# Optimization experiments

Measured on AMD Instinct MI355X. Metric: run time of the kernel, lower is better.

Reference implementation:

```python
import jax, jax.numpy as jnp
import numpy as np

# ---- init_kwargs-derived constants ----
B, IN_F, OUT_F = 8192, 4096, 4096
W_SCALE = 0.01          # layer_params['w_scale']
B_SCALE = 0.01          # layer_params['b_scale']
IN_MIN, IN_MAX = -1.0, 1.0   # input_stats
NUM_BITS = 8
QMAX = 2 ** NUM_BITS - 1
IN_SCALE = (IN_MAX - IN_MIN) / QMAX
IN_ZP = int(round(-IN_MIN / (IN_SCALE + 1e-12)))


def setup_inputs() -> dict:
    key = jax.random.key(0)
    k1, k2, k3 = jax.random.split(key, 3)
    x_float = jax.random.normal(k1, (B, IN_F), dtype=jnp.float32)
    # int8-range weights/bias (stored as int32 containers)
    w_q = jax.random.randint(k2, (OUT_F, IN_F), -128, 128, dtype=jnp.int32)
    b_q = jax.random.randint(k3, (OUT_F,), -128, 128, dtype=jnp.int32)
    return {"x_float": x_float, "w_q": w_q, "b_q": b_q}


def reference(x_float, w_q, b_q):
    # quantize input to uint8 range [0,255]
    x_q = jnp.clip(jnp.round(x_float / IN_SCALE + IN_ZP), 0, 255).astype(jnp.int32)
    x_shifted = x_q - IN_ZP                       # [B, IN_F] int32
    # exact int32 accumulation matmul: [B, IN_F] @ [IN_F, OUT_F]
    acc_int = jnp.matmul(x_shifted, w_q.T, preferred_element_type=jnp.int32)
    out = acc_int.astype(jnp.float32) * (IN_SCALE * W_SCALE)
    out = out + b_q.astype(jnp.float32) * B_SCALE  # bias_float = b_q * b_scale
    return out
```

## Files before the change

### kernel.cpp

```cpp
#include <hip/hip_runtime.h>
#include <stdint.h>

constexpr int Mdim = 8192;
constexpr int Ndim = 4096;
constexpr int Kdim = 4096;
constexpr int NT = Kdim / 128;

#define ISF        ((float)(2.0 / 255.0))
#define OUT_SCALE  ((float)(2.0 / 255.0 * 0.01))
#define BSCALE     0.01f

typedef int i32x4 __attribute__((ext_vector_type(4)));

__global__ __launch_bounds__(256) void quantize_x(const float* __restrict__ x,
                                                  int* __restrict__ x8,
                                                  int ngroups) {
  int idx = blockIdx.x * 256 + threadIdx.x;
  int stride = gridDim.x * 256;
  for (int g = idx; g < ngroups; g += stride) {
    float4 v = reinterpret_cast<const float4*>(x)[g];
    int a0 = (int)rintf(v.x / ISF + 127.0f);
    int a1 = (int)rintf(v.y / ISF + 127.0f);
    int a2 = (int)rintf(v.z / ISF + 127.0f);
    int a3 = (int)rintf(v.w / ISF + 127.0f);
    a0 = a0 < 0 ? 0 : (a0 > 255 ? 255 : a0); a0 -= 128;
    a1 = a1 < 0 ? 0 : (a1 > 255 ? 255 : a1); a1 -= 128;
    a2 = a2 < 0 ? 0 : (a2 > 255 ? 255 : a2); a2 -= 128;
    a3 = a3 < 0 ? 0 : (a3 > 255 ? 255 : a3); a3 -= 128;
    x8[g] = (a0 & 0xff) | ((a1 & 0xff) << 8) | ((a2 & 0xff) << 16) |
            (int)(((unsigned)(a3 & 0xff)) << 24);
  }
}

__global__ __launch_bounds__(256) void convert_w(const int* __restrict__ wq,
                                                 int* __restrict__ w8,
                                                 int* __restrict__ wsum) {
  int row = blockIdx.x;
  const int4* src = reinterpret_cast<const int4*>(wq + (size_t)row * Kdim);
  int* dst = w8 + (size_t)row * (Kdim / 4);
  int s = 0;
#pragma unroll
  for (int i = 0; i < 4; ++i) {
    int idx = i * 256 + threadIdx.x;
    int4 v = src[idx];
    s += v.x + v.y + v.z + v.w;
    dst[idx] = (v.x & 0xff) | ((v.y & 0xff) << 8) | ((v.z & 0xff) << 16) |
               (int)(((unsigned)(v.w & 0xff)) << 24);
  }
  __shared__ int red[256];
  red[threadIdx.x] = s;
  __syncthreads();
  for (int off = 128; off; off >>= 1) {
    if ((int)threadIdx.x < off) red[threadIdx.x] += red[threadIdx.x + off];
    __syncthreads();
  }
  if (threadIdx.x == 0) wsum[row] = red[0];
}

#define AS1C const __attribute__((address_space(1))) void*
#define AS3  __attribute__((address_space(3))) void*
#define GLL(src, dst) __builtin_amdgcn_global_load_lds((AS1C)(src), (AS3)(dst), 16, 0, 0)
#define BAR() asm volatile("s_barrier" ::: "memory")
#define MFMA(a, b, c) __builtin_amdgcn_mfma_i32_16x16x64_i8(a, b, c, 0, 0, 0)

__global__ __launch_bounds__(512) void gemm_i8_8ph(const int8_t* __restrict__ A8,
                                                   const int8_t* __restrict__ B8,
                                                   const int* __restrict__ wsum,
                                                   const int* __restrict__ bq,
                                                   float* __restrict__ out) {
  __shared__ uint8_t lds[131072];

  int bid = blockIdx.x;
  int wg = (bid & 7) * 64 + (bid >> 3);
  int bm = wg >> 4;
  int bn = wg & 15;

  const int tid = threadIdx.x;
  const int lane = tid & 63;
  const int wv = tid >> 6;
  const int wr = wv >> 2;
  const int wc = wv & 3;
  const int l15 = lane & 15, hi = lane >> 4;

  const int r3 = lane >> 3, s3 = lane & 7;
  const int swcol = (s3 ^ r3) << 4;
  const size_t aoff = (size_t)(bm * 256 + wv * 8 + r3) * Kdim + swcol;
  const size_t boff = (size_t)(bn * 256 + wv * 8 + r3) * Kdim + swcol;
  const int ldsw = wv * 1024;

#define ISSUE_A(P, t, half) do { \
    GLL(A8 + aoff + (size_t)(t) * 128 + (size_t)((half) * 128) * Kdim, \
        &lds[(P) * 32768 + (half) * 16384 + ldsw]); \
    GLL(A8 + aoff + (size_t)(t) * 128 + (size_t)((half) * 128 + 64) * Kdim, \
        &lds[(P) * 32768 + (half) * 16384 + 8192 + ldsw]); \
  } while (0)
#define ISSUE_B(P, t, half) do { \
    GLL(B8 + boff + (size_t)(t) * 128 + (size_t)((half) * 128) * Kdim, \
        &lds[65536 + (P) * 32768 + (half) * 16384 + ldsw]); \
    GLL(B8 + boff + (size_t)(t) * 128 + (size_t)((half) * 128 + 64) * Kdim, \
        &lds[65536 + (P) * 32768 + (half) * 16384 + 8192 + ldsw]); \
  } while (0)

  const int aRow = (wr * 128 + l15) * 128;
  const int bRow = (wc * 64 + l15) * 128;
  const int sl0 = (hi ^ (l15 & 7)) << 4;
  const int sl1 = ((4 + hi) ^ (l15 & 7)) << 4;

#define LDA(P, i, ks) (*reinterpret_cast<const i32x4*>( \
    &lds[(P) * 32768 + aRow + (i) * 2048 + ((ks) ? sl1 : sl0)]))
#define LDB(P, j, ks) (*reinterpret_cast<const i32x4*>( \
    &lds[65536 + (P) * 32768 + bRow + (j) * 2048 + ((ks) ? sl1 : sl0)]))

  i32x4 acc[8][4];
#pragma unroll
  for (int i = 0; i < 8; ++i)
#pragma unroll
    for (int j = 0; j < 4; ++j) acc[i][j] = (i32x4){0, 0, 0, 0};

  ISSUE_A(0, 0, 0); ISSUE_A(0, 0, 1);
  ISSUE_B(0, 0, 0); ISSUE_B(0, 0, 1);
  ISSUE_A(1, 1, 0); ISSUE_A(1, 1, 1);
  asm volatile("s_waitcnt vmcnt(4)" ::: "memory");
  BAR();

#define KTILE(P, t, DOB, DOA, VM4, VM0) do { \
    i32x4 a0[8], a1[8], bb0, bb1; \
     \
    if (DOB) ISSUE_B((P) ^ 1, (t) + 1, 0); \
    bb0 = LDB(P, 0, 0); bb1 = LDB(P, 1, 0); \
    _Pragma("unroll") for (int i = 0; i < 8; ++i) a0[i] = LDA(P, i, 0); \
    BAR(); __builtin_amdgcn_s_setprio(1); \
    _Pragma("unroll") for (int i = 0; i < 8; ++i) { \
      acc[i][0] = MFMA(a0[i], bb0, acc[i][0]); acc[i][1] = MFMA(a0[i], bb1, acc[i][1]); } \
    __builtin_amdgcn_s_setprio(0); BAR(); \
     \
    if (DOB) ISSUE_B((P) ^ 1, (t) + 1, 1); \
    bb0 = LDB(P, 2, 0); bb1 = LDB(P, 3, 0); \
    _Pragma("unroll") for (int i = 0; i < 8; ++i) a1[i] = LDA(P, i, 1); \
    BAR(); __builtin_amdgcn_s_setprio(1); \
    _Pragma("unroll") for (int i = 0; i < 8; ++i) { \
      acc[i][2] = MFMA(a0[i], bb0, acc[i][2]); acc[i][3] = MFMA(a0[i], bb1, acc[i][3]); } \
    __builtin_amdgcn_s_setprio(0); BAR(); \
     \
    if (DOA) ISSUE_A(P, (t) + 2, 0); \
    bb0 = LDB(P, 0, 1); bb1 = LDB(P, 1, 1); \
    BAR(); __builtin_amdgcn_s_setprio(1); \
    _Pragma("unroll") for (int i = 0; i < 8; ++i) { \
      acc[i][0] = MFMA(a1[i], bb0, acc[i][0]); acc[i][1] = MFMA(a1[i], bb1, acc[i][1]); } \
    __builtin_amdgcn_s_setprio(0); BAR(); \
     \
    if (DOA) ISSUE_A(P, (t) + 2, 1); \
    bb0 = LDB(P, 2, 1); bb1 = LDB(P, 3, 1); \
    BAR(); __builtin_amdgcn_s_setprio(1); \
    _Pragma("unroll") for (int i = 0; i < 8; ++i) { \
      acc[i][2] = MFMA(a1[i], bb0, acc[i][2]); acc[i][3] = MFMA(a1[i], bb1, acc[i][3]); } \
    __builtin_amdgcn_s_setprio(0); \
    if (VM4) asm volatile("s_waitcnt vmcnt(4)" ::: "memory"); \
    if (VM0) asm volatile("s_waitcnt vmcnt(0)" ::: "memory"); \
    BAR(); \
  } while (0)

  for (int it = 0; it < NT / 2 - 1; ++it) {
    int ta = 2 * it, tb = 2 * it + 1;
    KTILE(0, ta, 1, 1, 1, 0);
    KTILE(1, tb, 1, 1, 1, 0);
  }
  KTILE(0, 30, 1, 0, 0, 1);
  KTILE(1, 31, 0, 0, 0, 0);

#pragma unroll
  for (int j = 0; j < 4; ++j) {
    int col = bn * 256 + wc * 64 + j * 16 + l15;
    float fb = (float)bq[col] * BSCALE;
    int ws = wsum[col];
#pragma unroll
    for (int i = 0; i < 8; ++i) {
      int rbase = bm * 256 + wr * 128 + i * 16 + hi * 4;
#pragma unroll
      for (int p = 0; p < 4; ++p)
        out[(size_t)(rbase + p) * Ndim + col] = (float)(acc[i][j][p] + ws) * OUT_SCALE + fb;
    }
  }
#undef KTILE
#undef ISSUE_A
#undef ISSUE_B
#undef LDA
#undef LDB
}

__global__ void fallback_kernel(const float* __restrict__ x, const int* __restrict__ wq,
                                const int* __restrict__ bq, float* __restrict__ out) {
  int col = blockIdx.x * 16 + (threadIdx.x & 15);
  int row = blockIdx.y * 16 + (threadIdx.x >> 4);
  const float* xr = x + (size_t)row * Kdim;
  const int* wr_ = wq + (size_t)col * Kdim;
  int acc = 0;
  for (int k = 0; k < Kdim; ++k) {
    int v = (int)rintf(xr[k] / ISF + 127.0f);
    v = v < 0 ? 0 : (v > 255 ? 255 : v);
    acc += (v - 127) * wr_[k];
  }
  out[(size_t)row * Ndim + col] = (float)acc * OUT_SCALE + (float)bq[col] * BSCALE;
}

extern "C" void kernel_launch(void* const* d_in, const int* in_sizes, int n_in,
                              void* d_out, int out_size, void* d_ws, size_t ws_size,
                              hipStream_t stream) {
  const float* x = (const float*)d_in[0];
  const int* wq = (const int*)d_in[1];
  const int* bq = (const int*)d_in[2];
  float* out = (float*)d_out;

  const size_t x8_bytes = (size_t)Mdim * Kdim;
  const size_t w8_bytes = (size_t)Ndim * Kdim;
  const size_t ws_need = x8_bytes + w8_bytes + (size_t)Ndim * sizeof(int);

  if (ws_size >= ws_need) {
    int8_t* x8 = (int8_t*)d_ws;
    int8_t* w8 = x8 + x8_bytes;
    int* wsum = (int*)(w8 + w8_bytes);

    quantize_x<<<2048, 256, 0, stream>>>(x, (int*)x8, Mdim * Kdim / 4);
    convert_w<<<Ndim, 256, 0, stream>>>(wq, (int*)w8, wsum);
    gemm_i8_8ph<<<(Mdim / 256) * (Ndim / 256), 512, 0, stream>>>(x8, w8, wsum, bq, out);
  } else {
    dim3 grid(Ndim / 16, Mdim / 16);
    fallback_kernel<<<grid, 256, 0, stream>>>(x, wq, bq, out);
  }
}
```

Before: 179.2 us.

## Switch int8 GEMM to 32x32x32 MFMA tiles with A/B prefetch roles swapped

Replaces the 16x16x64 int8 MFMA with the 32x32x32 variant, so each wave computes 4x2 32x32 tiles instead of 8x4 16x16 tiles. This cuts the number of MFMA issues and LDS fragment loads per K step. The prefetch schedule is also reordered: the next A tile goes to the other buffer and B is refilled two tiles ahead, and a min-blocks launch bound of 2 is added. The epilogue is rewritten for the 32x32 output layout, which gives a different store pattern and a new LDS swizzle indexing across four K sub-steps.

```diff
diff --git a/kernel.cpp b/kernel.cpp
--- a/kernel.cpp
+++ b/kernel.cpp
@@ -11,6 +11,7 @@
 #define BSCALE     0.01f
 
 typedef int i32x4 __attribute__((ext_vector_type(4)));
+typedef int i32x16 __attribute__((ext_vector_type(16)));
 
 __global__ __launch_bounds__(256) void quantize_x(const float* __restrict__ x,
                                                   int* __restrict__ x8,
@@ -61,13 +62,13 @@
 #define AS3  __attribute__((address_space(3))) void*
 #define GLL(src, dst) __builtin_amdgcn_global_load_lds((AS1C)(src), (AS3)(dst), 16, 0, 0)
 #define BAR() asm volatile("s_barrier" ::: "memory")
-#define MFMA(a, b, c) __builtin_amdgcn_mfma_i32_16x16x64_i8(a, b, c, 0, 0, 0)
-
-__global__ __launch_bounds__(512) void gemm_i8_8ph(const int8_t* __restrict__ A8,
-                                                   const int8_t* __restrict__ B8,
-                                                   const int* __restrict__ wsum,
-                                                   const int* __restrict__ bq,
-                                                   float* __restrict__ out) {
+#define MFMA32(a, b, c) __builtin_amdgcn_mfma_i32_32x32x32_i8(a, b, c, 0, 0, 0)
+
+__global__ __launch_bounds__(512, 2) void gemm_i8_32(const int8_t* __restrict__ A8,
+                                                     const int8_t* __restrict__ B8,
+                                                     const int* __restrict__ wsum,
+                                                     const int* __restrict__ bq,
+                                                     float* __restrict__ out) {
   __shared__ uint8_t lds[131072];
 
   int bid = blockIdx.x;
@@ -80,7 +81,8 @@
   const int wv = tid >> 6;
   const int wr = wv >> 2;
   const int wc = wv & 3;
-  const int l15 = lane & 15, hi = lane >> 4;
+  const int l31 = lane & 31, hi1 = lane >> 5;
+  const int sw = l31 & 7;
 
   const int r3 = lane >> 3, s3 = lane & 7;
   const int swcol = (s3 ^ r3) << 4;
@@ -101,59 +103,71 @@
         &lds[65536 + (P) * 32768 + (half) * 16384 + 8192 + ldsw]); \
   } while (0)
 
-  const int aRow = (wr * 128 + l15) * 128;
-  const int bRow = (wc * 64 + l15) * 128;
-  const int sl0 = (hi ^ (l15 & 7)) << 4;
-  const int sl1 = ((4 + hi) ^ (l15 & 7)) << 4;
-
-#define LDA(P, i, ks) (*reinterpret_cast<const i32x4*>( \
-    &lds[(P) * 32768 + aRow + (i) * 2048 + ((ks) ? sl1 : sl0)]))
-#define LDB(P, j, ks) (*reinterpret_cast<const i32x4*>( \
-    &lds[65536 + (P) * 32768 + bRow + (j) * 2048 + ((ks) ? sl1 : sl0)]))
-
-  i32x4 acc[8][4];
-#pragma unroll
-  for (int i = 0; i < 8; ++i)
-#pragma unroll
-    for (int j = 0; j < 4; ++j) acc[i][j] = (i32x4){0, 0, 0, 0};
+  int arow[4], brow[2], sl[4];
+#pragma unroll
+  for (int ri = 0; ri < 4; ++ri) arow[ri] = (wr * 128 + ri * 32 + l31) * 128;
+#pragma unroll
+  for (int cj = 0; cj < 2; ++cj) brow[cj] = (wc * 64 + cj * 32 + l31) * 128;
+#pragma unroll
+  for (int ks = 0; ks < 4; ++ks) sl[ks] = ((ks * 2 + hi1) ^ sw) << 4;
+
+#define LDA(P, ri, ks) (*reinterpret_cast<const i32x4*>(&lds[(P) * 32768 + arow[ri] + sl[ks]]))
+#define LDB(P, cj, ks) (*reinterpret_cast<const i32x4*>(&lds[65536 + (P) * 32768 + brow[cj] + sl[ks]]))
+
+  i32x16 acc[4][2];
+#pragma unroll
+  for (int i = 0; i < 4; ++i)
+#pragma unroll
+    for (int j = 0; j < 2; ++j)
+#pragma unroll
+      for (int p = 0; p < 16; ++p) acc[i][j][p] = 0;
 
   ISSUE_A(0, 0, 0); ISSUE_A(0, 0, 1);
   ISSUE_B(0, 0, 0); ISSUE_B(0, 0, 1);
-  ISSUE_A(1, 1, 0); ISSUE_A(1, 1, 1);
+  ISSUE_B(1, 1, 0); ISSUE_B(1, 1, 1);
   asm volatile("s_waitcnt vmcnt(4)" ::: "memory");
   BAR();
 
-#define KTILE(P, t, DOB, DOA, VM4, VM0) do { \
-    i32x4 a0[8], a1[8], bb0, bb1; \
-     \
-    if (DOB) ISSUE_B((P) ^ 1, (t) + 1, 0); \
-    bb0 = LDB(P, 0, 0); bb1 = LDB(P, 1, 0); \
-    _Pragma("unroll") for (int i = 0; i < 8; ++i) a0[i] = LDA(P, i, 0); \
-    BAR(); __builtin_amdgcn_s_setprio(1); \
-    _Pragma("unroll") for (int i = 0; i < 8; ++i) { \
-      acc[i][0] = MFMA(a0[i], bb0, acc[i][0]); acc[i][1] = MFMA(a0[i], bb1, acc[i][1]); } \
+#define PH_MFMA(AV, BK) do { \
+    acc[0][0] = MFMA32(AV[0], b_[0][BK], acc[0][0]); \
+    acc[0][1] = MFMA32(AV[0], b_[1][BK], acc[0][1]); \
+    acc[1][0] = MFMA32(AV[1], b_[0][BK], acc[1][0]); \
+    acc[1][1] = MFMA32(AV[1], b_[1][BK], acc[1][1]); \
+    acc[2][0] = MFMA32(AV[2], b_[0][BK], acc[2][0]); \
+    acc[2][1] = MFMA32(AV[2], b_[1][BK], acc[2][1]); \
+    acc[3][0] = MFMA32(AV[3], b_[0][BK], acc[3][0]); \
+    acc[3][1] = MFMA32(AV[3], b_[1][BK], acc[3][1]); \
+  } while (0)
+
+#define KTILE(P, t, DOA, DOB, VM4, VM0) do { \
+    i32x4 a_[4], b_[2][4]; \
+     \
+    if (DOA) ISSUE_A((P) ^ 1, (t) + 1, 0); \
+    b_[0][0] = LDB(P, 0, 0); b_[1][0] = LDB(P, 1, 0); \
+    b_[0][1] = LDB(P, 0, 1); b_[1][1] = LDB(P, 1, 1); \
+    a_[0] = LDA(P, 0, 0); a_[1] = LDA(P, 1, 0); a_[2] = LDA(P, 2, 0); a_[3] = LDA(P, 3, 0); \
+    BAR(); __builtin_amdgcn_s_setprio(1); \
+    PH_MFMA(a_, 0); \
     __builtin_amdgcn_s_setprio(0); BAR(); \
      \
-    if (DOB) ISSUE_B((P) ^ 1, (t) + 1, 1); \
-    bb0 = LDB(P, 2, 0); bb1 = LDB(P, 3, 0); \
-    _Pragma("unroll") for (int i = 0; i < 8; ++i) a1[i] = LDA(P, i, 1); \
-    BAR(); __builtin_amdgcn_s_setprio(1); \
-    _Pragma("unroll") for (int i = 0; i < 8; ++i) { \
-      acc[i][2] = MFMA(a0[i], bb0, acc[i][2]); acc[i][3] = MFMA(a0[i], bb1, acc[i][3]); } \
+    if (DOA) ISSUE_A((P) ^ 1, (t) + 1, 1); \
+    b_[0][2] = LDB(P, 0, 2); b_[1][2] = LDB(P, 1, 2); \
+    b_[0][3] = LDB(P, 0, 3); b_[1][3] = LDB(P, 1, 3); \
+    a_[0] = LDA(P, 0, 1); a_[1] = LDA(P, 1, 1); a_[2] = LDA(P, 2, 1); a_[3] = LDA(P, 3, 1); \
+    BAR(); __builtin_amdgcn_s_setprio(1); \
+    PH_MFMA(a_, 1); \
     __builtin_amdgcn_s_setprio(0); BAR(); \
      \
-    if (DOA) ISSUE_A(P, (t) + 2, 0); \
-    bb0 = LDB(P, 0, 1); bb1 = LDB(P, 1, 1); \
-    BAR(); __builtin_amdgcn_s_setprio(1); \
-    _Pragma("unroll") for (int i = 0; i < 8; ++i) { \
-      acc[i][0] = MFMA(a1[i], bb0, acc[i][0]); acc[i][1] = MFMA(a1[i], bb1, acc[i][1]); } \
+    if (DOB) ISSUE_B(P, (t) + 2, 0); \
+    a_[0] = LDA(P, 0, 2); a_[1] = LDA(P, 1, 2); a_[2] = LDA(P, 2, 2); a_[3] = LDA(P, 3, 2); \
+    BAR(); __builtin_amdgcn_s_setprio(1); \
+    PH_MFMA(a_, 2); \
     __builtin_amdgcn_s_setprio(0); BAR(); \
      \
-    if (DOA) ISSUE_A(P, (t) + 2, 1); \
-    bb0 = LDB(P, 2, 1); bb1 = LDB(P, 3, 1); \
-    BAR(); __builtin_amdgcn_s_setprio(1); \
-    _Pragma("unroll") for (int i = 0; i < 8; ++i) { \
-      acc[i][2] = MFMA(a1[i], bb0, acc[i][2]); acc[i][3] = MFMA(a1[i], bb1, acc[i][3]); } \
+    if (DOB) ISSUE_B(P, (t) + 2, 1); \
+    a_[0] = LDA(P, 0, 3); a_[1] = LDA(P, 1, 3); a_[2] = LDA(P, 2, 3); a_[3] = LDA(P, 3, 3); \
+    BAR(); __builtin_amdgcn_s_setprio(1); \
+    PH_MFMA(a_, 3); \
     __builtin_amdgcn_s_setprio(0); \
     if (VM4) asm volatile("s_waitcnt vmcnt(4)" ::: "memory"); \
     if (VM0) asm volatile("s_waitcnt vmcnt(0)" ::: "memory"); \
@@ -161,27 +175,29 @@
   } while (0)
 
   for (int it = 0; it < NT / 2 - 1; ++it) {
-    int ta = 2 * it, tb = 2 * it + 1;
-    KTILE(0, ta, 1, 1, 1, 0);
-    KTILE(1, tb, 1, 1, 1, 0);
+    KTILE(0, 2 * it, 1, 1, 1, 0);
+    KTILE(1, 2 * it + 1, 1, 1, 1, 0);
   }
   KTILE(0, 30, 1, 0, 0, 1);
   KTILE(1, 31, 0, 0, 0, 0);
 
 #pragma unroll
-  for (int j = 0; j < 4; ++j) {
-    int col = bn * 256 + wc * 64 + j * 16 + l15;
+  for (int cj = 0; cj < 2; ++cj) {
+    int col = bn * 256 + wc * 64 + cj * 32 + l31;
     float fb = (float)bq[col] * BSCALE;
     int ws = wsum[col];
 #pragma unroll
-    for (int i = 0; i < 8; ++i) {
-      int rbase = bm * 256 + wr * 128 + i * 16 + hi * 4;
-#pragma unroll
-      for (int p = 0; p < 4; ++p)
-        out[(size_t)(rbase + p) * Ndim + col] = (float)(acc[i][j][p] + ws) * OUT_SCALE + fb;
+    for (int ri = 0; ri < 4; ++ri) {
+      int rb = bm * 256 + wr * 128 + ri * 32 + hi1 * 4;
+#pragma unroll
+      for (int p = 0; p < 16; ++p) {
+        int row = rb + (p & 3) + 8 * (p >> 2);
+        out[(size_t)row * Ndim + col] = (float)(acc[ri][cj][p] + ws) * OUT_SCALE + fb;
+      }
     }
   }
 #undef KTILE
+#undef PH_MFMA
 #undef ISSUE_A
 #undef ISSUE_B
 #undef LDA
@@ -222,7 +238,7 @@
 
     quantize_x<<<2048, 256, 0, stream>>>(x, (int*)x8, Mdim * Kdim / 4);
     convert_w<<<Ndim, 256, 0, stream>>>(wq, (int*)w8, wsum);
-    gemm_i8_8ph<<<(Mdim / 256) * (Ndim / 256), 512, 0, stream>>>(x8, w8, wsum, bq, out);
+    gemm_i8_32<<<(Mdim / 256) * (Ndim / 256), 512, 0, stream>>>(x8, w8, wsum, bq, out);
   } else {
     dim3 grid(Ndim / 16, Mdim / 16);
     fallback_kernel<<<grid, 256, 0, stream>>>(x, wq, bq, out);
```

Result: slower. 193.4 us (+7.9%).

## Software-pipeline LDS fragment loads across MFMA phases and tiles

Applied to the files above, without the earlier changes.

Restructures the int8 GEMM main loop so that each phase's LDS reads for the next B/A fragments are issued before the current phase's MFMAs, and the first fragments of the next K-tile are prefetched inside the last phase. This cuts the barrier count per tile and moves both A-half global-to-LDS issues to the end of the tile, aiming to hide LDS latency behind matrix work. It also adds a min-blocks-per-CU hint of 2 to the launch bounds. With 128 KB of shared memory per block two blocks may not fit on a CU anyway, and the hint could cap registers enough to spill the large accumulator and fragment arrays.

```diff
diff --git a/kernel.cpp b/kernel.cpp
--- a/kernel.cpp
+++ b/kernel.cpp
@@ -61,13 +61,14 @@
 #define AS3  __attribute__((address_space(3))) void*
 #define GLL(src, dst) __builtin_amdgcn_global_load_lds((AS1C)(src), (AS3)(dst), 16, 0, 0)
 #define BAR() asm volatile("s_barrier" ::: "memory")
+#define VMC(N) asm volatile("s_waitcnt vmcnt(" #N ")" ::: "memory")
 #define MFMA(a, b, c) __builtin_amdgcn_mfma_i32_16x16x64_i8(a, b, c, 0, 0, 0)
 
-__global__ __launch_bounds__(512) void gemm_i8_8ph(const int8_t* __restrict__ A8,
-                                                   const int8_t* __restrict__ B8,
-                                                   const int* __restrict__ wsum,
-                                                   const int* __restrict__ bq,
-                                                   float* __restrict__ out) {
+__global__ __launch_bounds__(512, 2) void gemm_i8_pl(const int8_t* __restrict__ A8,
+                                                     const int8_t* __restrict__ B8,
+                                                     const int* __restrict__ wsum,
+                                                     const int* __restrict__ bq,
+                                                     float* __restrict__ out) {
   __shared__ uint8_t lds[131072];
 
   int bid = blockIdx.x;
@@ -117,56 +118,66 @@
 #pragma unroll
     for (int j = 0; j < 4; ++j) acc[i][j] = (i32x4){0, 0, 0, 0};
 
+  i32x4 a0[8], a1[8], b1_[2], b2_[2], b3_[2], b4_[2];
+
   ISSUE_A(0, 0, 0); ISSUE_A(0, 0, 1);
   ISSUE_B(0, 0, 0); ISSUE_B(0, 0, 1);
   ISSUE_A(1, 1, 0); ISSUE_A(1, 1, 1);
-  asm volatile("s_waitcnt vmcnt(4)" ::: "memory");
+  VMC(4);
   BAR();
-
-#define KTILE(P, t, DOB, DOA, VM4, VM0) do { \
-    i32x4 a0[8], a1[8], bb0, bb1; \
+#pragma unroll
+  for (int i = 0; i < 8; ++i) a0[i] = LDA(0, i, 0);
+  b1_[0] = LDB(0, 0, 0); b1_[1] = LDB(0, 1, 0);
+
+#define TILE(P, t, DOB, DOA, VM4, VM0, CROSS) do { \
      \
     if (DOB) ISSUE_B((P) ^ 1, (t) + 1, 0); \
-    bb0 = LDB(P, 0, 0); bb1 = LDB(P, 1, 0); \
-    _Pragma("unroll") for (int i = 0; i < 8; ++i) a0[i] = LDA(P, i, 0); \
-    BAR(); __builtin_amdgcn_s_setprio(1); \
-    _Pragma("unroll") for (int i = 0; i < 8; ++i) { \
-      acc[i][0] = MFMA(a0[i], bb0, acc[i][0]); acc[i][1] = MFMA(a0[i], bb1, acc[i][1]); } \
-    __builtin_amdgcn_s_setprio(0); BAR(); \
+    BAR(); \
+    b2_[0] = LDB(P, 2, 0); b2_[1] = LDB(P, 3, 0); \
+    __builtin_amdgcn_s_setprio(1); \
+    _Pragma("unroll") for (int i = 0; i < 8; ++i) { \
+      acc[i][0] = MFMA(a0[i], b1_[0], acc[i][0]); \
+      acc[i][1] = MFMA(a0[i], b1_[1], acc[i][1]); } \
+    __builtin_amdgcn_s_setprio(0); \
      \
     if (DOB) ISSUE_B((P) ^ 1, (t) + 1, 1); \
-    bb0 = LDB(P, 2, 0); bb1 = LDB(P, 3, 0); \
+    BAR(); \
     _Pragma("unroll") for (int i = 0; i < 8; ++i) a1[i] = LDA(P, i, 1); \
-    BAR(); __builtin_amdgcn_s_setprio(1); \
-    _Pragma("unroll") for (int i = 0; i < 8; ++i) { \
-      acc[i][2] = MFMA(a0[i], bb0, acc[i][2]); acc[i][3] = MFMA(a0[i], bb1, acc[i][3]); } \
-    __builtin_amdgcn_s_setprio(0); BAR(); \
-     \
-    if (DOA) ISSUE_A(P, (t) + 2, 0); \
-    bb0 = LDB(P, 0, 1); bb1 = LDB(P, 1, 1); \
-    BAR(); __builtin_amdgcn_s_setprio(1); \
-    _Pragma("unroll") for (int i = 0; i < 8; ++i) { \
-      acc[i][0] = MFMA(a1[i], bb0, acc[i][0]); acc[i][1] = MFMA(a1[i], bb1, acc[i][1]); } \
-    __builtin_amdgcn_s_setprio(0); BAR(); \
-     \
-    if (DOA) ISSUE_A(P, (t) + 2, 1); \
-    bb0 = LDB(P, 2, 1); bb1 = LDB(P, 3, 1); \
-    BAR(); __builtin_amdgcn_s_setprio(1); \
-    _Pragma("unroll") for (int i = 0; i < 8; ++i) { \
-      acc[i][2] = MFMA(a1[i], bb0, acc[i][2]); acc[i][3] = MFMA(a1[i], bb1, acc[i][3]); } \
-    __builtin_amdgcn_s_setprio(0); \
-    if (VM4) asm volatile("s_waitcnt vmcnt(4)" ::: "memory"); \
-    if (VM0) asm volatile("s_waitcnt vmcnt(0)" ::: "memory"); \
-    BAR(); \
+    b3_[0] = LDB(P, 0, 1); b3_[1] = LDB(P, 1, 1); \
+    __builtin_amdgcn_s_setprio(1); \
+    _Pragma("unroll") for (int i = 0; i < 8; ++i) { \
+      acc[i][2] = MFMA(a0[i], b2_[0], acc[i][2]); \
+      acc[i][3] = MFMA(a0[i], b2_[1], acc[i][3]); } \
+    __builtin_amdgcn_s_setprio(0); \
+     \
+    BAR(); \
+    b4_[0] = LDB(P, 2, 1); b4_[1] = LDB(P, 3, 1); \
+    __builtin_amdgcn_s_setprio(1); \
+    _Pragma("unroll") for (int i = 0; i < 8; ++i) { \
+      acc[i][0] = MFMA(a1[i], b3_[0], acc[i][0]); \
+      acc[i][1] = MFMA(a1[i], b3_[1], acc[i][1]); } \
+    __builtin_amdgcn_s_setprio(0); \
+     \
+    if (DOA) { ISSUE_A(P, (t) + 2, 0); ISSUE_A(P, (t) + 2, 1); } \
+    if (VM4) VMC(4); \
+    if (VM0) VMC(0); \
+    BAR(); \
+    if (CROSS) { \
+      _Pragma("unroll") for (int i = 0; i < 8; ++i) a0[i] = LDA((P) ^ 1, i, 0); \
+      b1_[0] = LDB((P) ^ 1, 0, 0); b1_[1] = LDB((P) ^ 1, 1, 0); } \
+    __builtin_amdgcn_s_setprio(1); \
+    _Pragma("unroll") for (int i = 0; i < 8; ++i) { \
+      acc[i][2] = MFMA(a1[i], b4_[0], acc[i][2]); \
+      acc[i][3] = MFMA(a1[i], b4_[1], acc[i][3]); } \
+    __builtin_amdgcn_s_setprio(0); \
   } while (0)
 
   for (int it = 0; it < NT / 2 - 1; ++it) {
-    int ta = 2 * it, tb = 2 * it + 1;
-    KTILE(0, ta, 1, 1, 1, 0);
-    KTILE(1, tb, 1, 1, 1, 0);
-  }
-  KTILE(0, 30, 1, 0, 0, 1);
-  KTILE(1, 31, 0, 0, 0, 0);
+    TILE(0, 2 * it, 1, 1, 1, 0, 1);
+    TILE(1, 2 * it + 1, 1, 1, 1, 0, 1);
+  }
+  TILE(0, 30, 1, 0, 0, 1, 1);
+  TILE(1, 31, 0, 0, 0, 0, 0);
 
 #pragma unroll
   for (int j = 0; j < 4; ++j) {
@@ -181,7 +192,7 @@
         out[(size_t)(rbase + p) * Ndim + col] = (float)(acc[i][j][p] + ws) * OUT_SCALE + fb;
     }
   }
-#undef KTILE
+#undef TILE
 #undef ISSUE_A
 #undef ISSUE_B
 #undef LDA
@@ -222,7 +233,7 @@
 
     quantize_x<<<2048, 256, 0, stream>>>(x, (int*)x8, Mdim * Kdim / 4);
     convert_w<<<Ndim, 256, 0, stream>>>(wq, (int*)w8, wsum);
-    gemm_i8_8ph<<<(Mdim / 256) * (Ndim / 256), 512, 0, stream>>>(x8, w8, wsum, bq, out);
+    gemm_i8_pl<<<(Mdim / 256) * (Ndim / 256), 512, 0, stream>>>(x8, w8, wsum, bq, out);
   } else {
     dim3 grid(Ndim / 16, Mdim / 16);
     fallback_kernel<<<grid, 256, 0, stream>>>(x, wq, bq, out);
```

After: 242.3 us. +35.2%, slower.

## Triple-buffer A tiles in LDS and restructure MFMA phases for register reuse

Applied to the files above, without the earlier changes.

Grows the LDS tile to 160KB with three A buffers and two B buffers, so A prefetch runs two tiles ahead with a rotating buffer schedule unrolled over six tiles. Each phase now loads four B fragments and four A fragments and issues a 4x4 MFMA block, halving A register pressure. It also adds an explicit lgkmcnt(0) wait with a sched_barrier before each MFMA group. The aim is to hide more global-load latency and cut register use, at the cost of more LDS, which rules out a second workgroup per CU despite the launch bound of 2, and of stricter waits that serialise LDS reads with compute.

```diff
diff --git a/kernel.cpp b/kernel.cpp
--- a/kernel.cpp
+++ b/kernel.cpp
@@ -61,14 +61,18 @@
 #define AS3  __attribute__((address_space(3))) void*
 #define GLL(src, dst) __builtin_amdgcn_global_load_lds((AS1C)(src), (AS3)(dst), 16, 0, 0)
 #define BAR() asm volatile("s_barrier" ::: "memory")
+#define LGK0() do { asm volatile("s_waitcnt lgkmcnt(0)" ::: "memory"); \
+                    __builtin_amdgcn_sched_barrier(0); } while (0)
+#define VMC(N) asm volatile("s_waitcnt vmcnt(" #N ")" ::: "memory")
 #define MFMA(a, b, c) __builtin_amdgcn_mfma_i32_16x16x64_i8(a, b, c, 0, 0, 0)
-
-__global__ __launch_bounds__(512) void gemm_i8_8ph(const int8_t* __restrict__ A8,
-                                                   const int8_t* __restrict__ B8,
-                                                   const int* __restrict__ wsum,
-                                                   const int* __restrict__ bq,
-                                                   float* __restrict__ out) {
-  __shared__ uint8_t lds[131072];
+#define BBASE 98304
+
+__global__ __launch_bounds__(512, 2) void gemm_i8_q(const int8_t* __restrict__ A8,
+                                                    const int8_t* __restrict__ B8,
+                                                    const int* __restrict__ wsum,
+                                                    const int* __restrict__ bq,
+                                                    float* __restrict__ out) {
+  __shared__ uint8_t lds[163840];
 
   int bid = blockIdx.x;
   int wg = (bid & 7) * 64 + (bid >> 3);
@@ -96,9 +100,9 @@
   } while (0)
 #define ISSUE_B(P, t, half) do { \
     GLL(B8 + boff + (size_t)(t) * 128 + (size_t)((half) * 128) * Kdim, \
-        &lds[65536 + (P) * 32768 + (half) * 16384 + ldsw]); \
+        &lds[BBASE + (P) * 32768 + (half) * 16384 + ldsw]); \
     GLL(B8 + boff + (size_t)(t) * 128 + (size_t)((half) * 128 + 64) * Kdim, \
-        &lds[65536 + (P) * 32768 + (half) * 16384 + 8192 + ldsw]); \
+        &lds[BBASE + (P) * 32768 + (half) * 16384 + 8192 + ldsw]); \
   } while (0)
 
   const int aRow = (wr * 128 + l15) * 128;
@@ -109,7 +113,7 @@
 #define LDA(P, i, ks) (*reinterpret_cast<const i32x4*>( \
     &lds[(P) * 32768 + aRow + (i) * 2048 + ((ks) ? sl1 : sl0)]))
 #define LDB(P, j, ks) (*reinterpret_cast<const i32x4*>( \
-    &lds[65536 + (P) * 32768 + bRow + (j) * 2048 + ((ks) ? sl1 : sl0)]))
+    &lds[BBASE + (P) * 32768 + bRow + (j) * 2048 + ((ks) ? sl1 : sl0)]))
 
   i32x4 acc[8][4];
 #pragma unroll
@@ -120,53 +124,61 @@
   ISSUE_A(0, 0, 0); ISSUE_A(0, 0, 1);
   ISSUE_B(0, 0, 0); ISSUE_B(0, 0, 1);
   ISSUE_A(1, 1, 0); ISSUE_A(1, 1, 1);
-  asm volatile("s_waitcnt vmcnt(4)" ::: "memory");
+  VMC(4);
   BAR();
 
-#define KTILE(P, t, DOB, DOA, VM4, VM0) do { \
-    i32x4 a0[8], a1[8], bb0, bb1; \
-     \
-    if (DOB) ISSUE_B((P) ^ 1, (t) + 1, 0); \
-    bb0 = LDB(P, 0, 0); bb1 = LDB(P, 1, 0); \
-    _Pragma("unroll") for (int i = 0; i < 8; ++i) a0[i] = LDA(P, i, 0); \
-    BAR(); __builtin_amdgcn_s_setprio(1); \
-    _Pragma("unroll") for (int i = 0; i < 8; ++i) { \
-      acc[i][0] = MFMA(a0[i], bb0, acc[i][0]); acc[i][1] = MFMA(a0[i], bb1, acc[i][1]); } \
+#define TILE(TA, TB, TA2, t, DOB, DOA, VM4, VM0) do { \
+    i32x4 a_[4], B0[4], B1[4]; \
+     \
+    if (DOB) ISSUE_B((TB) ^ 1, (t) + 1, 0); \
+    B0[0] = LDB(TB, 0, 0); B0[1] = LDB(TB, 1, 0); B0[2] = LDB(TB, 2, 0); B0[3] = LDB(TB, 3, 0); \
+    a_[0] = LDA(TA, 0, 0); a_[1] = LDA(TA, 1, 0); a_[2] = LDA(TA, 2, 0); a_[3] = LDA(TA, 3, 0); \
+    BAR(); LGK0(); __builtin_amdgcn_s_setprio(1); \
+    _Pragma("unroll") for (int i = 0; i < 4; ++i) \
+      _Pragma("unroll") for (int j = 0; j < 4; ++j) \
+        acc[i][j] = MFMA(a_[i], B0[j], acc[i][j]); \
     __builtin_amdgcn_s_setprio(0); BAR(); \
      \
-    if (DOB) ISSUE_B((P) ^ 1, (t) + 1, 1); \
-    bb0 = LDB(P, 2, 0); bb1 = LDB(P, 3, 0); \
-    _Pragma("unroll") for (int i = 0; i < 8; ++i) a1[i] = LDA(P, i, 1); \
-    BAR(); __builtin_amdgcn_s_setprio(1); \
-    _Pragma("unroll") for (int i = 0; i < 8; ++i) { \
-      acc[i][2] = MFMA(a0[i], bb0, acc[i][2]); acc[i][3] = MFMA(a0[i], bb1, acc[i][3]); } \
+    if (DOB) ISSUE_B((TB) ^ 1, (t) + 1, 1); \
+    a_[0] = LDA(TA, 4, 0); a_[1] = LDA(TA, 5, 0); a_[2] = LDA(TA, 6, 0); a_[3] = LDA(TA, 7, 0); \
+    BAR(); LGK0(); __builtin_amdgcn_s_setprio(1); \
+    _Pragma("unroll") for (int i = 0; i < 4; ++i) \
+      _Pragma("unroll") for (int j = 0; j < 4; ++j) \
+        acc[i + 4][j] = MFMA(a_[i], B0[j], acc[i + 4][j]); \
     __builtin_amdgcn_s_setprio(0); BAR(); \
      \
-    if (DOA) ISSUE_A(P, (t) + 2, 0); \
-    bb0 = LDB(P, 0, 1); bb1 = LDB(P, 1, 1); \
-    BAR(); __builtin_amdgcn_s_setprio(1); \
-    _Pragma("unroll") for (int i = 0; i < 8; ++i) { \
-      acc[i][0] = MFMA(a1[i], bb0, acc[i][0]); acc[i][1] = MFMA(a1[i], bb1, acc[i][1]); } \
+    if (DOA) ISSUE_A(TA2, (t) + 2, 0); \
+    B1[0] = LDB(TB, 0, 1); B1[1] = LDB(TB, 1, 1); B1[2] = LDB(TB, 2, 1); B1[3] = LDB(TB, 3, 1); \
+    a_[0] = LDA(TA, 0, 1); a_[1] = LDA(TA, 1, 1); a_[2] = LDA(TA, 2, 1); a_[3] = LDA(TA, 3, 1); \
+    BAR(); LGK0(); __builtin_amdgcn_s_setprio(1); \
+    _Pragma("unroll") for (int i = 0; i < 4; ++i) \
+      _Pragma("unroll") for (int j = 0; j < 4; ++j) \
+        acc[i][j] = MFMA(a_[i], B1[j], acc[i][j]); \
     __builtin_amdgcn_s_setprio(0); BAR(); \
      \
-    if (DOA) ISSUE_A(P, (t) + 2, 1); \
-    bb0 = LDB(P, 2, 1); bb1 = LDB(P, 3, 1); \
-    BAR(); __builtin_amdgcn_s_setprio(1); \
-    _Pragma("unroll") for (int i = 0; i < 8; ++i) { \
-      acc[i][2] = MFMA(a1[i], bb0, acc[i][2]); acc[i][3] = MFMA(a1[i], bb1, acc[i][3]); } \
+    if (DOA) ISSUE_A(TA2, (t) + 2, 1); \
+    a_[0] = LDA(TA, 4, 1); a_[1] = LDA(TA, 5, 1); a_[2] = LDA(TA, 6, 1); a_[3] = LDA(TA, 7, 1); \
+    BAR(); LGK0(); __builtin_amdgcn_s_setprio(1); \
+    _Pragma("unroll") for (int i = 0; i < 4; ++i) \
+      _Pragma("unroll") for (int j = 0; j < 4; ++j) \
+        acc[i + 4][j] = MFMA(a_[i], B1[j], acc[i + 4][j]); \
     __builtin_amdgcn_s_setprio(0); \
-    if (VM4) asm volatile("s_waitcnt vmcnt(4)" ::: "memory"); \
-    if (VM0) asm volatile("s_waitcnt vmcnt(0)" ::: "memory"); \
+    if (VM4) VMC(4); \
+    if (VM0) VMC(0); \
     BAR(); \
   } while (0)
 
-  for (int it = 0; it < NT / 2 - 1; ++it) {
-    int ta = 2 * it, tb = 2 * it + 1;
-    KTILE(0, ta, 1, 1, 1, 0);
-    KTILE(1, tb, 1, 1, 1, 0);
-  }
-  KTILE(0, 30, 1, 0, 0, 1);
-  KTILE(1, 31, 0, 0, 0, 0);
+  for (int it = 0; it < 5; ++it) {
+    int t = it * 6;
+    TILE(0, 0, 2, t + 0, 1, 1, 1, 0);
+    TILE(1, 1, 0, t + 1, 1, 1, 1, 0);
+    TILE(2, 0, 1, t + 2, 1, 1, 1, 0);
+    TILE(0, 1, 2, t + 3, 1, 1, 1, 0);
+    TILE(1, 0, 0, t + 4, 1, 1, 1, 0);
+    TILE(2, 1, 1, t + 5, 1, 1, 1, 0);
+  }
+  TILE(0, 0, 2, 30, 1, 0, 0, 1);
+  TILE(1, 1, 0, 31, 0, 0, 0, 0);
 
 #pragma unroll
   for (int j = 0; j < 4; ++j) {
@@ -181,7 +193,7 @@
         out[(size_t)(rbase + p) * Ndim + col] = (float)(acc[i][j][p] + ws) * OUT_SCALE + fb;
     }
   }
-#undef KTILE
+#undef TILE
 #undef ISSUE_A
 #undef ISSUE_B
 #undef LDA
@@ -222,7 +234,7 @@
 
     quantize_x<<<2048, 256, 0, stream>>>(x, (int*)x8, Mdim * Kdim / 4);
     convert_w<<<Ndim, 256, 0, stream>>>(wq, (int*)w8, wsum);
-    gemm_i8_8ph<<<(Mdim / 256) * (Ndim / 256), 512, 0, stream>>>(x8, w8, wsum, bq, out);
+    gemm_i8_q<<<(Mdim / 256) * (Ndim / 256), 512, 0, stream>>>(x8, w8, wsum, bq, out);
   } else {
     dim3 grid(Ndim / 16, Mdim / 16);
     fallback_kernel<<<grid, 256, 0, stream>>>(x, wq, bq, out);
```

After: 182.0 us. No clear change (+1.5%).
